# Kernel optimization log

Measured on AMD Instinct MI355X. Metric: run time of the kernel, lower is better.

Reference implementation:

```python
import jax, jax.numpy as jnp
import numpy as np

B, S, QD, KD = 8, 8192, 1024, 1024
AD = min(QD, KD)
EPS = 1e-5


def _ste(x, xq):
    # straight-through estimator: forward uses xq, gradient flows as identity
    return x + jax.lax.stop_gradient(xq - x)


def bitlinear(x, w, b):
    """BitNet b1.58-style BitLinear: ternary per-tensor weight quant,
    per-token int8 absmax activation quant, both with STE."""
    s = jnp.mean(jnp.abs(w)) + EPS                      # per-tensor weight scale
    wq = _ste(w, jnp.clip(jnp.round(w / s), -1.0, 1.0) * s)
    g = jnp.max(jnp.abs(x), axis=-1, keepdims=True) + EPS  # per-token act scale
    xq = _ste(x, jnp.clip(jnp.round(x * (127.0 / g)), -128.0, 127.0) * (g / 127.0))
    return jnp.matmul(xq, wq.T) + b


def setup_inputs() -> dict:
    key = jax.random.key(0)
    ks = jax.random.split(key, 6)
    sc = 0.02
    return {
        "query": jax.random.normal(ks[0], (B, QD), dtype=jnp.float32),
        "context_memory": jax.random.normal(ks[1], (B, S, KD), dtype=jnp.float32),
        "w_q": jax.random.normal(ks[2], (AD, QD), dtype=jnp.float32) * sc,
        "b_q": jnp.zeros((AD,), dtype=jnp.float32),
        "w_k": jax.random.normal(ks[3], (AD, KD), dtype=jnp.float32) * sc,
        "b_k": jnp.zeros((AD,), dtype=jnp.float32),
        "w_v": jax.random.normal(ks[4], (QD, KD), dtype=jnp.float32) * sc,
        "b_v": jnp.zeros((QD,), dtype=jnp.float32),
        "w_c": jax.random.normal(ks[5], (QD, 2 * QD), dtype=jnp.float32) * sc,
        "b_c": jnp.zeros((QD,), dtype=jnp.float32),
    }


def reference(query, context_memory, w_q, b_q, w_k, b_k, w_v, b_v, w_c, b_c):
    attention_dim = w_q.shape[0]
    q = bitlinear(query, w_q, b_q)                 # [B, A]
    k = bitlinear(context_memory, w_k, b_k)        # [B, S, A]
    v = bitlinear(context_memory, w_v, b_v)        # [B, S, QD]
    scores = jnp.einsum('ba,bsa->bs', q, k) / (attention_dim ** 0.5)
    attn = jax.nn.softmax(scores, axis=-1)         # [B, S]
    ctx = jnp.einsum('bs,bsq->bq', attn, v)        # [B, QD]
    combined = jnp.concatenate([query, ctx], axis=-1)  # [B, 2*QD]
    return bitlinear(combined, w_c, b_c)           # [B, QD]
```

## Files before the change

### kernel.cpp

```cpp
#include <hip/hip_runtime.h>
#include <hip/hip_bf16.h>
#include <math.h>

#define EPS 1e-5f

static constexpr int Bb = 8;
static constexpr int Ss = 8192;
static constexpr int Dd = 1024;
static constexpr int NW = 64;
static constexpr int NWv = NW * 4;
static constexpr int TOK = Ss / NWv;
static constexpr int NPAIR = TOK / 2;
static constexpr int NCH = 64;
static constexpr int RC = Dd / NCH;


__device__ __forceinline__ float blk_reduce(float v, bool ismax, volatile float* lds) {
#pragma unroll
  for (int msk = 32; msk; msk >>= 1) {
    float o = __shfl_xor(v, msk);
    v = ismax ? fmaxf(v, o) : (v + o);
  }
  int w = threadIdx.x >> 6;
  __syncthreads();
  if ((threadIdx.x & 63) == 0) lds[w] = v;
  __syncthreads();
  return ismax ? fmaxf(fmaxf(lds[0], lds[1]), fmaxf(lds[2], lds[3]))
               : (lds[0] + lds[1] + lds[2] + lds[3]);
}

__device__ __forceinline__ float wred_sum(float v) {
#pragma unroll
  for (int msk = 32; msk; msk >>= 1) v += __shfl_xor(v, msk);
  return v;
}

__device__ __forceinline__ float quantf(float x, float c) {
  return fminf(fmaxf(rintf(x * c), -128.f), 127.f);
}

__device__ __forceinline__ float ternf(float w, float s) {
  return fminf(fmaxf(rintf(w / s), -1.f), 1.f);
}

__device__ __forceinline__ float4 tern4(float4 w, float s) {
  return make_float4(ternf(w.x, s), ternf(w.y, s), ternf(w.z, s), ternf(w.w, s));
}

__device__ __forceinline__ float4 quant4(float4 v, float c) {
  return make_float4(quantf(v.x, c), quantf(v.y, c), quantf(v.z, c), quantf(v.w, c));
}

__device__ __forceinline__ float absmax4(float4 v) {
  return fmaxf(fmaxf(fabsf(v.x), fabsf(v.y)), fmaxf(fabsf(v.z), fabsf(v.w)));
}


__global__ __launch_bounds__(256) void k_scales(
    const float* __restrict__ w0, const float* __restrict__ w1,
    const float* __restrict__ w2, const float* __restrict__ w3,
    double* __restrict__ part, float* __restrict__ scales, int* __restrict__ cnt)
{
  int seg = blockIdx.x >> 6;
  int blk = blockIdx.x & 63;
  const float* w = seg == 0 ? w0 : seg == 1 ? w1 : seg == 2 ? w2 : w3;
  int n4 = (seg == 3 ? (1024 * 2048) : (1024 * 1024)) >> 2;
  const float4* w4 = (const float4*)w;
  double acc = 0.0;
  for (int i = blk * 256 + threadIdx.x; i < n4; i += 64 * 256) {
    float4 v = w4[i];
    acc += (double)fabsf(v.x) + (double)fabsf(v.y)
         + (double)fabsf(v.z) + (double)fabsf(v.w);
  }
  __shared__ double sred[256];
  sred[threadIdx.x] = acc;
  __syncthreads();
  for (int s = 128; s > 0; s >>= 1) {
    if (threadIdx.x < s) sred[threadIdx.x] += sred[threadIdx.x + s];
    __syncthreads();
  }
  __shared__ int lastold;
  if (threadIdx.x == 0) {
    part[blockIdx.x] = sred[0];
    __threadfence();
    lastold = atomicAdd(cnt, 1);
  }
  __syncthreads();
  if (lastold == 255) {
    __threadfence();
    if (threadIdx.x < 4) {
      int sg = threadIdx.x;
      double s = 0.0;
      for (int i = 0; i < 64; i++) s += part[sg * 64 + i];
      double n = (sg == 3) ? 2097152.0 : 1048576.0;
      scales[sg] = (float)(s / n) + EPS;
    }
  }
}


__global__ __launch_bounds__(256) void k_qgemv(
    const float* __restrict__ query, const float* __restrict__ W,
    const float* __restrict__ bias, const float* __restrict__ scales,
    float* __restrict__ out)
{
  __shared__ float cs[Dd];
  __shared__ float red[4];
  int b = blockIdx.x >> 8, grp = blockIdx.x & 255;
  int tid = threadIdx.x, wv = tid >> 6, lane = tid & 63;
  float4 v = ((const float4*)(query + (size_t)b * Dd))[tid];
  float am = blk_reduce(absmax4(v), true, red);
  float g = am + EPS;
  float c = 127.0f / g;
  ((float4*)cs)[tid] = quant4(v, c);
  __syncthreads();
  float s = scales[0];
  int o = grp * 4 + wv;
  const float4* wr = (const float4*)(W + (size_t)o * Dd);
  float acc = 0.f;
#pragma unroll
  for (int i = 0; i < 4; i++) {
    int idx = i * 64 + lane;
    float4 w4 = wr[idx];
    float4 a4 = ((const float4*)cs)[idx];
    acc += a4.x * ternf(w4.x, s) + a4.y * ternf(w4.y, s)
         + a4.z * ternf(w4.z, s) + a4.w * ternf(w4.w, s);
  }
  acc = wred_sum(acc);
  if (lane == 0) out[(size_t)b * Dd + o] = s * (g / 127.0f) * acc + bias[o];
}


__global__ __launch_bounds__(256) void k_qk(
    const float* __restrict__ q, const float* __restrict__ Wk,
    const float* __restrict__ bk, const float* __restrict__ scales,
    float* __restrict__ part, float* __restrict__ qk, float* __restrict__ qdotbk,
    int* __restrict__ cnt)
{
  __shared__ float qs[Bb * RC];
  int ch = blockIdx.x;
  int a0 = ch * RC;
  int tid = threadIdx.x;
  if (tid < Bb * RC) {
    int b = tid / RC, a = tid - b * RC;
    qs[tid] = q[(size_t)b * Dd + a0 + a];
  }
  __syncthreads();
  float s = scales[1];
  float4 acc[Bb];
#pragma unroll
  for (int b = 0; b < Bb; b++) acc[b] = make_float4(0.f, 0.f, 0.f, 0.f);
  const float4* Wr = (const float4*)(Wk + (size_t)a0 * Dd);
  for (int i = 0; i < RC; i++) {
    float4 t4 = tern4(Wr[(size_t)i * 256 + tid], s);
#pragma unroll
    for (int b = 0; b < Bb; b++) {
      float qb = qs[b * RC + i];
      acc[b].x += qb * t4.x; acc[b].y += qb * t4.y;
      acc[b].z += qb * t4.z; acc[b].w += qb * t4.w;
    }
  }
#pragma unroll
  for (int b = 0; b < Bb; b++)
    ((float4*)part)[((size_t)ch * Bb + b) * 256 + tid] = acc[b];

  __threadfence();
  if (tid == 0) {
    atomicAdd(cnt, 1);
    while (__hip_atomic_load(cnt, __ATOMIC_ACQUIRE, __HIP_MEMORY_SCOPE_AGENT) < NCH)
      __builtin_amdgcn_s_sleep(8);
  }
  __syncthreads();
  __threadfence();

  int b = blockIdx.x >> 3, dc = blockIdx.x & 7;
  if (tid < 32) {
    int d4 = dc * 32 + tid;
    float4 a = make_float4(0.f, 0.f, 0.f, 0.f);
    for (int k = 0; k < NCH; k++) {
      float4 p = ((const float4*)part)[((size_t)k * Bb + b) * 256 + d4];
      a.x += p.x; a.y += p.y; a.z += p.z; a.w += p.w;
    }
    ((float4*)qk)[(size_t)b * 256 + d4] = make_float4(s * a.x, s * a.y, s * a.z, s * a.w);
  } else if (dc == 0 && tid >= 64 && tid < 128) {
    int lane = tid - 64;
    float p = 0.f;
    for (int a2 = lane; a2 < Dd; a2 += 64) p += q[(size_t)b * Dd + a2] * bk[a2];
    p = wred_sum(p);
    if (lane == 0) qdotbk[b] = p;
  }
}


__global__ __launch_bounds__(256) void k_pass(
    const float* __restrict__ X, const float* __restrict__ qk,
    const float* __restrict__ qdotbk,
    float* __restrict__ m_part, float* __restrict__ l_part,
    float* __restrict__ t_part)
{
  int b    = blockIdx.x >> 6;
  int wg   = blockIdx.x & 63;
  int wv   = threadIdx.x >> 6;
  int lane = threadIdx.x & 63;
  int widx = wg * 4 + wv;
  int s0   = widx * TOK;

  const float4* qkb = (const float4*)(qk + (size_t)b * Dd);
  float4 qv0 = qkb[lane], qv1 = qkb[64 + lane], qv2 = qkb[128 + lane], qv3 = qkb[192 + lane];
  float qb = qdotbk[b];
  const float4* Xw = (const float4*)(X + ((size_t)b * Ss + s0) * Dd);

  float m = -INFINITY, l = 0.f;
  float4 a0 = make_float4(0,0,0,0), a1 = a0, a2 = a0, a3 = a0;

  float4 xA0 = Xw[lane],       xA1 = Xw[64 + lane],  xA2 = Xw[128 + lane], xA3 = Xw[192 + lane];
  float4 xB0 = Xw[256 + lane], xB1 = Xw[320 + lane], xB2 = Xw[384 + lane], xB3 = Xw[448 + lane];

  for (int p = 0; p < NPAIR; p++) {
    size_t nb = (size_t)((p + 1 < NPAIR) ? p + 1 : p) * 512;
    float4 nA0 = Xw[nb + lane],       nA1 = Xw[nb + 64 + lane],
           nA2 = Xw[nb + 128 + lane], nA3 = Xw[nb + 192 + lane];
    float4 nB0 = Xw[nb + 256 + lane], nB1 = Xw[nb + 320 + lane],
           nB2 = Xw[nb + 384 + lane], nB3 = Xw[nb + 448 + lane];

    float amA = fmaxf(fmaxf(absmax4(xA0), absmax4(xA1)), fmaxf(absmax4(xA2), absmax4(xA3)));
    float amB = fmaxf(fmaxf(absmax4(xB0), absmax4(xB1)), fmaxf(absmax4(xB2), absmax4(xB3)));
#pragma unroll
    for (int msk = 32; msk; msk >>= 1) {
      float oA = __shfl_xor(amA, msk);
      float oB = __shfl_xor(amB, msk);
      amA = fmaxf(amA, oA);
      amB = fmaxf(amB, oB);
    }
    float gA = amA + EPS, gB = amB + EPS;
    float cA = 127.0f / gA, cB = 127.0f / gB;
    float giA = gA / 127.0f, giB = gB / 127.0f;

    float qA00 = quantf(xA0.x, cA), qA01 = quantf(xA0.y, cA), qA02 = quantf(xA0.z, cA), qA03 = quantf(xA0.w, cA);
    float qA10 = quantf(xA1.x, cA), qA11 = quantf(xA1.y, cA), qA12 = quantf(xA1.z, cA), qA13 = quantf(xA1.w, cA);
    float qA20 = quantf(xA2.x, cA), qA21 = quantf(xA2.y, cA), qA22 = quantf(xA2.z, cA), qA23 = quantf(xA2.w, cA);
    float qA30 = quantf(xA3.x, cA), qA31 = quantf(xA3.y, cA), qA32 = quantf(xA3.z, cA), qA33 = quantf(xA3.w, cA);
    float qB00 = quantf(xB0.x, cB), qB01 = quantf(xB0.y, cB), qB02 = quantf(xB0.z, cB), qB03 = quantf(xB0.w, cB);
    float qB10 = quantf(xB1.x, cB), qB11 = quantf(xB1.y, cB), qB12 = quantf(xB1.z, cB), qB13 = quantf(xB1.w, cB);
    float qB20 = quantf(xB2.x, cB), qB21 = quantf(xB2.y, cB), qB22 = quantf(xB2.z, cB), qB23 = quantf(xB2.w, cB);
    float qB30 = quantf(xB3.x, cB), qB31 = quantf(xB3.y, cB), qB32 = quantf(xB3.z, cB), qB33 = quantf(xB3.w, cB);

    float dtA = qA00 * qv0.x + qA01 * qv0.y + qA02 * qv0.z + qA03 * qv0.w
              + qA10 * qv1.x + qA11 * qv1.y + qA12 * qv1.z + qA13 * qv1.w
              + qA20 * qv2.x + qA21 * qv2.y + qA22 * qv2.z + qA23 * qv2.w
              + qA30 * qv3.x + qA31 * qv3.y + qA32 * qv3.z + qA33 * qv3.w;
    float dtB = qB00 * qv0.x + qB01 * qv0.y + qB02 * qv0.z + qB03 * qv0.w
              + qB10 * qv1.x + qB11 * qv1.y + qB12 * qv1.z + qB13 * qv1.w
              + qB20 * qv2.x + qB21 * qv2.y + qB22 * qv2.z + qB23 * qv2.w
              + qB30 * qv3.x + qB31 * qv3.y + qB32 * qv3.z + qB33 * qv3.w;
#pragma unroll
    for (int msk = 32; msk; msk >>= 1) {
      float oA = __shfl_xor(dtA, msk);
      float oB = __shfl_xor(dtB, msk);
      dtA += oA;
      dtB += oB;
    }

    float sA = (dtA * giA + qb) * 0.03125f;
    float sB = (dtB * giB + qb) * 0.03125f;

    float mn  = fmaxf(m, fmaxf(sA, sB));
    float scl = __expf(m - mn);
    float eA  = __expf(sA - mn);
    float eB  = __expf(sB - mn);
    l = l * scl + eA + eB;
    float cfA = eA * giA, cfB = eB * giB;
    a0.x = a0.x * scl + cfA * qA00 + cfB * qB00; a0.y = a0.y * scl + cfA * qA01 + cfB * qB01;
    a0.z = a0.z * scl + cfA * qA02 + cfB * qB02; a0.w = a0.w * scl + cfA * qA03 + cfB * qB03;
    a1.x = a1.x * scl + cfA * qA10 + cfB * qB10; a1.y = a1.y * scl + cfA * qA11 + cfB * qB11;
    a1.z = a1.z * scl + cfA * qA12 + cfB * qB12; a1.w = a1.w * scl + cfA * qA13 + cfB * qB13;
    a2.x = a2.x * scl + cfA * qA20 + cfB * qB20; a2.y = a2.y * scl + cfA * qA21 + cfB * qB21;
    a2.z = a2.z * scl + cfA * qA22 + cfB * qB22; a2.w = a2.w * scl + cfA * qA23 + cfB * qB23;
    a3.x = a3.x * scl + cfA * qA30 + cfB * qB30; a3.y = a3.y * scl + cfA * qA31 + cfB * qB31;
    a3.z = a3.z * scl + cfA * qA32 + cfB * qB32; a3.w = a3.w * scl + cfA * qA33 + cfB * qB33;
    m = mn;

    xA0 = nA0; xA1 = nA1; xA2 = nA2; xA3 = nA3;
    xB0 = nB0; xB1 = nB1; xB2 = nB2; xB3 = nB3;
  }

  size_t pidx = (size_t)b * NWv + widx;
  float4* tpw = (float4*)t_part + (size_t)pidx * 256;
  tpw[lane] = a0; tpw[64 + lane] = a1; tpw[128 + lane] = a2; tpw[192 + lane] = a3;
  if (lane == 0) { m_part[pidx] = m; l_part[pidx] = l; }
}


__global__ __launch_bounds__(256) void k_comb(
    const float* __restrict__ m_part, const float* __restrict__ l_part,
    const float* __restrict__ t_part, float* __restrict__ t16,
    float* __restrict__ t, int* __restrict__ cnt)
{
  __shared__ float red[4];
  int b = blockIdx.x >> 4, k = blockIdx.x & 15;
  int tid = threadIdx.x;
  float mi = m_part[(size_t)b * NWv + tid];
  float M = blk_reduce(mi, true, red);
  float li = l_part[(size_t)b * NWv + tid] * expf(mi - M);
  float L = blk_reduce(li, false, red);

  float4 acc = make_float4(0,0,0,0);
  for (int i = 0; i < 16; i++) {
    size_t pi = (size_t)b * NWv + k * 16 + i;
    float w = expf(m_part[pi] - M);
    float4 tp = ((const float4*)t_part)[pi * 256 + tid];
    acc.x += w * tp.x; acc.y += w * tp.y; acc.z += w * tp.z; acc.w += w * tp.w;
  }
  ((float4*)t16)[((size_t)(b * 16 + k)) * 256 + tid] = acc;

  __shared__ int lastold;
  if (tid == 0) {
    __threadfence();
    lastold = atomicAdd(&cnt[b], 1);
  }
  __syncthreads();
  if (lastold == 15) {
    __threadfence();
    float invL = 1.0f / L;
    float4 a = make_float4(0,0,0,0);
    for (int kk = 0; kk < 16; kk++) {
      float4 v = ((const float4*)t16)[((size_t)(b * 16 + kk)) * 256 + tid];
      a.x += v.x; a.y += v.y; a.z += v.z; a.w += v.w;
    }
    ((float4*)t)[(size_t)b * 256 + tid] =
        make_float4(a.x * invL, a.y * invL, a.z * invL, a.w * invL);
  }
}


__global__ __launch_bounds__(256) void k_tern_gemv_f32(
    const float* __restrict__ act, const float* __restrict__ W,
    const float* __restrict__ bias, const float* __restrict__ scales, int sidx,
    float* __restrict__ out, int K, int N)
{
  int wave = blockIdx.x * 4 + (threadIdx.x >> 6);
  int lane = threadIdx.x & 63;
  int b = wave / N, o = wave - b * N;
  float s = scales[sidx];
  const float4* wr = (const float4*)(W + (size_t)o * K);
  const float4* ar = (const float4*)(act + (size_t)b * K);
  int n4 = K >> 2;
  float acc = 0.f;
  for (int i = lane; i < n4; i += 64) {
    float4 w4 = wr[i];
    float4 a4 = ar[i];
    acc += a4.x * ternf(w4.x, s) + a4.y * ternf(w4.y, s)
         + a4.z * ternf(w4.z, s) + a4.w * ternf(w4.w, s);
  }
  acc = wred_sum(acc);
  if (lane == 0) out[(size_t)b * N + o] = s * acc + bias[o];
}


__global__ __launch_bounds__(256) void k_final(
    const float* __restrict__ query, const float* __restrict__ ctx,
    const float* __restrict__ W, const float* __restrict__ bias,
    const float* __restrict__ scales, float* __restrict__ out)
{
  __shared__ float cs[2 * Dd];
  __shared__ float red[4];
  int b = blockIdx.x >> 8, grp = blockIdx.x & 255;
  int tid = threadIdx.x, wv = tid >> 6, lane = tid & 63;
  float4 vq = ((const float4*)(query + (size_t)b * Dd))[tid];
  float4 vc = ((const float4*)(ctx   + (size_t)b * Dd))[tid];
  float am = blk_reduce(fmaxf(absmax4(vq), absmax4(vc)), true, red);
  float g = am + EPS;
  float c = 127.0f / g;
  ((float4*)cs)[tid]       = quant4(vq, c);
  ((float4*)cs)[256 + tid] = quant4(vc, c);
  __syncthreads();
  float s = scales[3];
  int o = grp * 4 + wv;
  const float4* wr = (const float4*)(W + (size_t)o * 2 * Dd);
  float acc = 0.f;
#pragma unroll
  for (int i = 0; i < 8; i++) {
    int idx = i * 64 + lane;
    float4 w4 = wr[idx];
    float4 a4 = ((const float4*)cs)[idx];
    acc += a4.x * ternf(w4.x, s) + a4.y * ternf(w4.y, s)
         + a4.z * ternf(w4.z, s) + a4.w * ternf(w4.w, s);
  }
  acc = wred_sum(acc);
  if (lane == 0) out[(size_t)b * Dd + o] = s * (g / 127.0f) * acc + bias[o];
}


extern "C" void kernel_launch(void* const* d_in, const int* in_sizes, int n_in,
                              void* d_out, int out_size, void* d_ws, size_t ws_size,
                              hipStream_t stream)
{
  const float* query = (const float*)d_in[0];
  const float* X     = (const float*)d_in[1];
  const float* w_q   = (const float*)d_in[2];
  const float* b_q   = (const float*)d_in[3];
  const float* w_k   = (const float*)d_in[4];
  const float* b_k   = (const float*)d_in[5];
  const float* w_v   = (const float*)d_in[6];
  const float* b_v   = (const float*)d_in[7];
  const float* w_c   = (const float*)d_in[8];
  const float* b_c   = (const float*)d_in[9];
  float* out = (float*)d_out;
  char* ws = (char*)d_ws;

  size_t off = 0;
  auto alloc = [&](size_t bytes) -> size_t {
    size_t o = off;
    off += (bytes + 255) & ~(size_t)255;
    return o;
  };
  size_t o_cnt    = alloc(256);
  size_t o_part   = alloc(256 * sizeof(double));
  size_t o_scales = alloc(4 * sizeof(float));
  size_t o_q      = alloc((size_t)Bb * Dd * 4);
  size_t o_qk     = alloc((size_t)Bb * Dd * 4);
  size_t o_qbk    = alloc(Bb * sizeof(float));
  size_t o_t      = alloc((size_t)Bb * Dd * 4);
  size_t o_ctx    = alloc((size_t)Bb * Dd * 4);
  size_t o_t16    = alloc((size_t)Bb * 16 * Dd * 4);
  size_t o_qkp    = alloc((size_t)NCH * Bb * Dd * 4);
  size_t o_mp     = alloc((size_t)Bb * NWv * 4);
  size_t o_lp     = alloc((size_t)Bb * NWv * 4);
  size_t o_tp     = alloc((size_t)Bb * NWv * Dd * 4);
  (void)ws_size;

  int*    cnt    = (int*)(ws + o_cnt);
  double* part   = (double*)(ws + o_part);
  float*  scales = (float*)(ws + o_scales);
  float*  qv     = (float*)(ws + o_q);
  float*  qk     = (float*)(ws + o_qk);
  float*  qbk    = (float*)(ws + o_qbk);
  float*  tvec   = (float*)(ws + o_t);
  float*  ctx    = (float*)(ws + o_ctx);
  float*  t16    = (float*)(ws + o_t16);
  float*  qkp    = (float*)(ws + o_qkp);
  float*  mp     = (float*)(ws + o_mp);
  float*  lp     = (float*)(ws + o_lp);
  float*  tp     = (float*)(ws + o_tp);

  hipMemsetAsync(ws + o_cnt, 0, 256, stream);
  k_scales<<<256, 256, 0, stream>>>(w_q, w_k, w_v, w_c, part, scales, &cnt[0]);
  k_qgemv<<<Bb * 256, 256, 0, stream>>>(query, w_q, b_q, scales, qv);
  k_qk<<<NCH, 256, 0, stream>>>(qv, w_k, b_k, scales, qkp, qk, qbk, &cnt[1]);
  k_pass<<<Bb * NW, 256, 0, stream>>>(X, qk, qbk, mp, lp, tp);
  k_comb<<<Bb * 16, 256, 0, stream>>>(mp, lp, tp, t16, tvec, &cnt[2]);
  k_tern_gemv_f32<<<(Bb * Dd) / 4, 256, 0, stream>>>(tvec, w_v, b_v, scales, 2, ctx, Dd, Dd);
  k_final<<<Bb * 256, 256, 0, stream>>>(query, ctx, w_c, b_c, scales, out);
}
```

Before: 134.7 us.

## Fuse query BitLinear GEMV into the q·Wk kernel per channel chunk

Removes the separate k_qgemv launch. Each of the 64 k_qk blocks now quantizes all 8 query rows into LDS and computes its own 16-row slice of q = BitLinear(query, w_q), keeping that slice in shared memory. It then feeds the slice straight into the ternary Wk projection, and the q·b_k dot is built from per-chunk partials. This saves a kernel launch and the global round trip of q. In exchange, each block redoes the query quantization, and only 64 blocks read w_q, so that work has less parallelism.

```diff
diff --git a/kernel.cpp b/kernel.cpp
--- a/kernel.cpp
+++ b/kernel.cpp
@@ -49,6 +49,10 @@
 
 __device__ __forceinline__ float4 quant4(float4 v, float c) {
   return make_float4(quantf(v.x, c), quantf(v.y, c), quantf(v.z, c), quantf(v.w, c));
+}
+
+__device__ __forceinline__ float dot4(float4 a, float4 b) {
+  return a.x * b.x + a.y * b.y + a.z * b.z + a.w * b.w;
 }
 
 __device__ __forceinline__ float absmax4(float4 v) {
@@ -99,70 +103,78 @@
 }
 
 
-__global__ __launch_bounds__(256) void k_qgemv(
-    const float* __restrict__ query, const float* __restrict__ W,
-    const float* __restrict__ bias, const float* __restrict__ scales,
-    float* __restrict__ out)
-{
-  __shared__ float cs[Dd];
+__global__ __launch_bounds__(256) void k_qk(
+    const float* __restrict__ query,
+    const float* __restrict__ w_q, const float* __restrict__ b_q,
+    const float* __restrict__ w_k, const float* __restrict__ b_k,
+    const float* __restrict__ scales,
+    float* __restrict__ part, float* __restrict__ qbk_part,
+    float* __restrict__ qk, float* __restrict__ qdotbk,
+    int* __restrict__ cnt)
+{
+  __shared__ float qs[Bb * Dd];
+  __shared__ float qs2[Bb * RC];
   __shared__ float red[4];
-  int b = blockIdx.x >> 8, grp = blockIdx.x & 255;
-  int tid = threadIdx.x, wv = tid >> 6, lane = tid & 63;
-  float4 v = ((const float4*)(query + (size_t)b * Dd))[tid];
-  float am = blk_reduce(absmax4(v), true, red);
-  float g = am + EPS;
-  float c = 127.0f / g;
-  ((float4*)cs)[tid] = quant4(v, c);
-  __syncthreads();
-  float s = scales[0];
-  int o = grp * 4 + wv;
-  const float4* wr = (const float4*)(W + (size_t)o * Dd);
-  float acc = 0.f;
-#pragma unroll
-  for (int i = 0; i < 4; i++) {
-    int idx = i * 64 + lane;
-    float4 w4 = wr[idx];
-    float4 a4 = ((const float4*)cs)[idx];
-    acc += a4.x * ternf(w4.x, s) + a4.y * ternf(w4.y, s)
-         + a4.z * ternf(w4.z, s) + a4.w * ternf(w4.w, s);
-  }
-  acc = wred_sum(acc);
-  if (lane == 0) out[(size_t)b * Dd + o] = s * (g / 127.0f) * acc + bias[o];
-}
-
-
-__global__ __launch_bounds__(256) void k_qk(
-    const float* __restrict__ q, const float* __restrict__ Wk,
-    const float* __restrict__ bk, const float* __restrict__ scales,
-    float* __restrict__ part, float* __restrict__ qk, float* __restrict__ qdotbk,
-    int* __restrict__ cnt)
-{
-  __shared__ float qs[Bb * RC];
+  __shared__ float gsh[8];
   int ch = blockIdx.x;
   int a0 = ch * RC;
-  int tid = threadIdx.x;
-  if (tid < Bb * RC) {
-    int b = tid / RC, a = tid - b * RC;
-    qs[tid] = q[(size_t)b * Dd + a0 + a];
-  }
-  __syncthreads();
-  float s = scales[1];
-  float4 acc[Bb];
-#pragma unroll
-  for (int b = 0; b < Bb; b++) acc[b] = make_float4(0.f, 0.f, 0.f, 0.f);
-  const float4* Wr = (const float4*)(Wk + (size_t)a0 * Dd);
+  int tid = threadIdx.x, wv = tid >> 6, lane = tid & 63;
+
+  for (int b = 0; b < 8; b++) {
+    float4 v = ((const float4*)(query + (size_t)b * Dd))[tid];
+    float am = blk_reduce(absmax4(v), true, red);
+    float g = am + EPS;
+    ((float4*)qs)[b * 256 + tid] = quant4(v, 127.0f / g);
+    if (tid == 0) gsh[b] = g;
+  }
+  __syncthreads();
+
+  float s0 = scales[0];
+  for (int r = 0; r < 4; r++) {
+    int row = a0 + wv * 4 + r;
+    const float4* wr = (const float4*)(w_q + (size_t)row * Dd);
+    float acc[8] = {0, 0, 0, 0, 0, 0, 0, 0};
+#pragma unroll
+    for (int i = 0; i < 4; i++) {
+      float4 t4 = tern4(wr[i * 64 + lane], s0);
+#pragma unroll
+      for (int b = 0; b < 8; b++)
+        acc[b] += dot4(((float4*)qs)[b * 256 + i * 64 + lane], t4);
+    }
+#pragma unroll
+    for (int b = 0; b < 8; b++) acc[b] = wred_sum(acc[b]);
+    if (lane == 0) {
+      float bq = b_q[row];
+#pragma unroll
+      for (int b = 0; b < 8; b++)
+        qs2[b * RC + wv * 4 + r] = s0 * (gsh[b] / 127.0f) * acc[b] + bq;
+    }
+  }
+  __syncthreads();
+
+  if (tid < 8) {
+    float p = 0.f;
+    for (int a = 0; a < RC; a++) p += qs2[tid * RC + a] * b_k[a0 + a];
+    qbk_part[ch * 8 + tid] = p;
+  }
+
+  float s1 = scales[1];
+  float4 acc4[Bb];
+#pragma unroll
+  for (int b = 0; b < Bb; b++) acc4[b] = make_float4(0.f, 0.f, 0.f, 0.f);
+  const float4* Wr = (const float4*)(w_k + (size_t)a0 * Dd);
   for (int i = 0; i < RC; i++) {
-    float4 t4 = tern4(Wr[(size_t)i * 256 + tid], s);
+    float4 t4 = tern4(Wr[(size_t)i * 256 + tid], s1);
 #pragma unroll
     for (int b = 0; b < Bb; b++) {
-      float qb = qs[b * RC + i];
-      acc[b].x += qb * t4.x; acc[b].y += qb * t4.y;
-      acc[b].z += qb * t4.z; acc[b].w += qb * t4.w;
+      float qb = qs2[b * RC + i];
+      acc4[b].x += qb * t4.x; acc4[b].y += qb * t4.y;
+      acc4[b].z += qb * t4.z; acc4[b].w += qb * t4.w;
     }
   }
 #pragma unroll
   for (int b = 0; b < Bb; b++)
-    ((float4*)part)[((size_t)ch * Bb + b) * 256 + tid] = acc[b];
+    ((float4*)part)[((size_t)ch * Bb + b) * 256 + tid] = acc4[b];
 
   __threadfence();
   if (tid == 0) {
@@ -181,13 +193,12 @@
       float4 p = ((const float4*)part)[((size_t)k * Bb + b) * 256 + d4];
       a.x += p.x; a.y += p.y; a.z += p.z; a.w += p.w;
     }
-    ((float4*)qk)[(size_t)b * 256 + d4] = make_float4(s * a.x, s * a.y, s * a.z, s * a.w);
+    ((float4*)qk)[(size_t)b * 256 + d4] = make_float4(s1 * a.x, s1 * a.y, s1 * a.z, s1 * a.w);
   } else if (dc == 0 && tid >= 64 && tid < 128) {
-    int lane = tid - 64;
-    float p = 0.f;
-    for (int a2 = lane; a2 < Dd; a2 += 64) p += q[(size_t)b * Dd + a2] * bk[a2];
+    int ch2 = tid - 64;
+    float p = qbk_part[ch2 * 8 + b];
     p = wred_sum(p);
-    if (lane == 0) qdotbk[b] = p;
+    if (ch2 == 0) qdotbk[b] = p;
   }
 }
 
@@ -417,9 +428,9 @@
   size_t o_cnt    = alloc(256);
   size_t o_part   = alloc(256 * sizeof(double));
   size_t o_scales = alloc(4 * sizeof(float));
-  size_t o_q      = alloc((size_t)Bb * Dd * 4);
   size_t o_qk     = alloc((size_t)Bb * Dd * 4);
   size_t o_qbk    = alloc(Bb * sizeof(float));
+  size_t o_qbkp   = alloc((size_t)NCH * Bb * 4);
   size_t o_t      = alloc((size_t)Bb * Dd * 4);
   size_t o_ctx    = alloc((size_t)Bb * Dd * 4);
   size_t o_t16    = alloc((size_t)Bb * 16 * Dd * 4);
@@ -432,9 +443,9 @@
   int*    cnt    = (int*)(ws + o_cnt);
   double* part   = (double*)(ws + o_part);
   float*  scales = (float*)(ws + o_scales);
-  float*  qv     = (float*)(ws + o_q);
   float*  qk     = (float*)(ws + o_qk);
   float*  qbk    = (float*)(ws + o_qbk);
+  float*  qbkp   = (float*)(ws + o_qbkp);
   float*  tvec   = (float*)(ws + o_t);
   float*  ctx    = (float*)(ws + o_ctx);
   float*  t16    = (float*)(ws + o_t16);
@@ -445,8 +456,8 @@
 
   hipMemsetAsync(ws + o_cnt, 0, 256, stream);
   k_scales<<<256, 256, 0, stream>>>(w_q, w_k, w_v, w_c, part, scales, &cnt[0]);
-  k_qgemv<<<Bb * 256, 256, 0, stream>>>(query, w_q, b_q, scales, qv);
-  k_qk<<<NCH, 256, 0, stream>>>(qv, w_k, b_k, scales, qkp, qk, qbk, &cnt[1]);
+  k_qk<<<NCH, 256, 0, stream>>>(query, w_q, b_q, w_k, b_k, scales,
+                                qkp, qbkp, qk, qbk, &cnt[1]);
   k_pass<<<Bb * NW, 256, 0, stream>>>(X, qk, qbk, mp, lp, tp);
   k_comb<<<Bb * 16, 256, 0, stream>>>(mp, lp, tp, t16, tvec, &cnt[2]);
   k_tern_gemv_f32<<<(Bb * Dd) / 4, 256, 0, stream>>>(tvec, w_v, b_v, scales, 2, ctx, Dd, Dd);
```

Result: slower. 139.7 us (+3.7%).

## Split qk kernel into partial and combine kernels, doubling chunk count

Applied to the files above, without the earlier changes.

The fused k_qk kernel, which used a grid-wide atomic spin barrier before reducing partials, is replaced by two launches: k_qk_part computes per-chunk partial products and k_qk_comb reduces them with 16-way parallelism per output through LDS. NCH goes from 64 to 128 so the partial stage spreads W_k reads over more blocks. The goal is to drop the spin-wait and the serial 64-step reduction done by only 32 threads per block, at the cost of one extra kernel launch and a larger partial buffer. The hardcoded tid>>3 indexing relies on RC being 8.

```diff
diff --git a/kernel.cpp b/kernel.cpp
--- a/kernel.cpp
+++ b/kernel.cpp
@@ -11,7 +11,7 @@
 static constexpr int NWv = NW * 4;
 static constexpr int TOK = Ss / NWv;
 static constexpr int NPAIR = TOK / 2;
-static constexpr int NCH = 64;
+static constexpr int NCH = 128;
 static constexpr int RC = Dd / NCH;
 
 
@@ -131,19 +131,16 @@
 }
 
 
-__global__ __launch_bounds__(256) void k_qk(
+__global__ __launch_bounds__(256) void k_qk_part(
     const float* __restrict__ q, const float* __restrict__ Wk,
-    const float* __restrict__ bk, const float* __restrict__ scales,
-    float* __restrict__ part, float* __restrict__ qk, float* __restrict__ qdotbk,
-    int* __restrict__ cnt)
-{
-  __shared__ float qs[Bb * RC];
-  int ch = blockIdx.x;
-  int a0 = ch * RC;
+    const float* __restrict__ scales, float* __restrict__ part)
+{
+  __shared__ float qs2[Bb * RC];
+  int ch = blockIdx.x, a0 = ch * RC;
   int tid = threadIdx.x;
   if (tid < Bb * RC) {
-    int b = tid / RC, a = tid - b * RC;
-    qs[tid] = q[(size_t)b * Dd + a0 + a];
+    int b = tid >> 3, a = tid & 7;
+    qs2[tid] = q[(size_t)b * Dd + a0 + a];
   }
   __syncthreads();
   float s = scales[1];
@@ -151,11 +148,12 @@
 #pragma unroll
   for (int b = 0; b < Bb; b++) acc[b] = make_float4(0.f, 0.f, 0.f, 0.f);
   const float4* Wr = (const float4*)(Wk + (size_t)a0 * Dd);
+#pragma unroll
   for (int i = 0; i < RC; i++) {
     float4 t4 = tern4(Wr[(size_t)i * 256 + tid], s);
 #pragma unroll
     for (int b = 0; b < Bb; b++) {
-      float qb = qs[b * RC + i];
+      float qb = qs2[b * RC + i];
       acc[b].x += qb * t4.x; acc[b].y += qb * t4.y;
       acc[b].z += qb * t4.z; acc[b].w += qb * t4.w;
     }
@@ -163,26 +161,39 @@
 #pragma unroll
   for (int b = 0; b < Bb; b++)
     ((float4*)part)[((size_t)ch * Bb + b) * 256 + tid] = acc[b];
-
-  __threadfence();
-  if (tid == 0) {
-    atomicAdd(cnt, 1);
-    while (__hip_atomic_load(cnt, __ATOMIC_ACQUIRE, __HIP_MEMORY_SCOPE_AGENT) < NCH)
-      __builtin_amdgcn_s_sleep(8);
-  }
-  __syncthreads();
-  __threadfence();
-
-  int b = blockIdx.x >> 3, dc = blockIdx.x & 7;
-  if (tid < 32) {
-    int d4 = dc * 32 + tid;
-    float4 a = make_float4(0.f, 0.f, 0.f, 0.f);
-    for (int k = 0; k < NCH; k++) {
-      float4 p = ((const float4*)part)[((size_t)k * Bb + b) * 256 + d4];
-      a.x += p.x; a.y += p.y; a.z += p.z; a.w += p.w;
-    }
-    ((float4*)qk)[(size_t)b * 256 + d4] = make_float4(s * a.x, s * a.y, s * a.z, s * a.w);
-  } else if (dc == 0 && tid >= 64 && tid < 128) {
+}
+
+
+__global__ __launch_bounds__(256) void k_qk_comb(
+    const float* __restrict__ part, const float* __restrict__ q,
+    const float* __restrict__ bk, const float* __restrict__ scales,
+    float* __restrict__ qk, float* __restrict__ qdotbk)
+{
+  __shared__ float4 lred[16][17];
+  int b = blockIdx.x >> 4, g = blockIdx.x & 15;
+  int tid = threadIdx.x;
+  int c = tid & 15, kg = tid >> 4;
+  int d4 = g * 16 + c;
+  float s = scales[1];
+  float4 a = make_float4(0.f, 0.f, 0.f, 0.f);
+#pragma unroll
+  for (int j = 0; j < NCH / 16; j++) {
+    int ch = kg * (NCH / 16) + j;
+    float4 p = ((const float4*)part)[((size_t)ch * Bb + b) * 256 + d4];
+    a.x += p.x; a.y += p.y; a.z += p.z; a.w += p.w;
+  }
+  lred[kg][c] = a;
+  __syncthreads();
+  if (kg == 0) {
+    float4 t = lred[0][c];
+#pragma unroll
+    for (int k = 1; k < 16; k++) {
+      float4 v = lred[k][c];
+      t.x += v.x; t.y += v.y; t.z += v.z; t.w += v.w;
+    }
+    ((float4*)qk)[(size_t)b * 256 + d4] =
+        make_float4(s * t.x, s * t.y, s * t.z, s * t.w);
+  } else if (g == 0 && tid >= 64 && tid < 128) {
     int lane = tid - 64;
     float p = 0.f;
     for (int a2 = lane; a2 < Dd; a2 += 64) p += q[(size_t)b * Dd + a2] * bk[a2];
@@ -446,7 +457,8 @@
   hipMemsetAsync(ws + o_cnt, 0, 256, stream);
   k_scales<<<256, 256, 0, stream>>>(w_q, w_k, w_v, w_c, part, scales, &cnt[0]);
   k_qgemv<<<Bb * 256, 256, 0, stream>>>(query, w_q, b_q, scales, qv);
-  k_qk<<<NCH, 256, 0, stream>>>(qv, w_k, b_k, scales, qkp, qk, qbk, &cnt[1]);
+  k_qk_part<<<NCH, 256, 0, stream>>>(qv, w_k, scales, qkp);
+  k_qk_comb<<<Bb * 16, 256, 0, stream>>>(qkp, qv, b_k, scales, qk, qbk);
   k_pass<<<Bb * NW, 256, 0, stream>>>(X, qk, qbk, mp, lp, tp);
   k_comb<<<Bb * 16, 256, 0, stream>>>(mp, lp, tp, t16, tvec, &cnt[2]);
   k_tern_gemv_f32<<<(Bb * Dd) / 4, 256, 0, stream>>>(tvec, w_v, b_v, scales, 2, ctx, Dd, Dd);
```

New measurement: 122.9 us. 1.1x faster.
